# Kernel tuning notes

Measured on AMD Instinct MI355X. Metric: run time of the kernel, lower is better.

The kernel has to match this reference:

```python
import jax, jax.numpy as jnp
import numpy as np

EMBED_DIM = 1024
NUM_HEADS = 16
HEAD_DIM = EMBED_DIM // NUM_HEADS


def setup_inputs() -> dict:
    key = jax.random.key(0)
    ks = jax.random.split(key, 9)
    B, S, D = 4, 2048, EMBED_DIM
    s = 1.0 / np.sqrt(D)
    inp = {
        "x": jax.random.normal(ks[0], (B, S, D), dtype=jnp.float32),
        "Wq": jax.random.uniform(ks[1], (D, D), jnp.float32, -s, s),
        "bq": jax.random.uniform(ks[2], (D,), jnp.float32, -s, s),
        "Wk": jax.random.uniform(ks[3], (D, D), jnp.float32, -s, s),
        "bk": jax.random.uniform(ks[4], (D,), jnp.float32, -s, s),
        "Wv": jax.random.uniform(ks[5], (D, D), jnp.float32, -s, s),
        "bv": jax.random.uniform(ks[6], (D,), jnp.float32, -s, s),
        "Wo": jax.random.uniform(ks[7], (D, D), jnp.float32, -s, s),
        "bo": jax.random.uniform(ks[8], (D,), jnp.float32, -s, s),
    }
    return inp


def reference(x, Wq, bq, Wk, bk, Wv, bv, Wo, bo):
    B, S, D = x.shape
    H, Hd = NUM_HEADS, HEAD_DIM
    scale = 1.0 / jnp.sqrt(jnp.asarray(Hd, x.dtype))

    def split_heads(t):  # (B,S,D) -> (B,H,S,Hd)
        return t.reshape(B, S, H, Hd).transpose(0, 2, 1, 3)

    q = split_heads(x @ Wq + bq)
    k = split_heads(x @ Wk + bk)
    v = split_heads(x @ Wv + bv)

    scores = jnp.einsum("bhqd,bhkd->bhqk", q, k) * scale
    attn = jax.nn.softmax(scores, axis=-1)  # dropout is identity in eval mode
    out = jnp.einsum("bhqk,bhkd->bhqd", attn, v)
    out = out.transpose(0, 2, 1, 3).reshape(B, S, D)
    return out @ Wo + bo
```

## Files before the change

### kernel.cpp

```cpp
#include <hip/hip_runtime.h>
#include <cstdint>

typedef unsigned short u16;
typedef uint32_t u32;
typedef float f32x4 __attribute__((ext_vector_type(4)));
typedef short s16x8 __attribute__((ext_vector_type(8)));
typedef u16 u16x4 __attribute__((ext_vector_type(4)));
typedef u32 u32x2 __attribute__((ext_vector_type(2)));
typedef u32 u32x4 __attribute__((ext_vector_type(4)));

__device__ __forceinline__ u16 f2bf(float f) {
  u32 u = __builtin_bit_cast(u32, f);
  u += 0x7FFFu + ((u >> 16) & 1u);
  return (u16)(u >> 16);
}

__device__ __forceinline__ u32 pack2bf_trunc(float lo, float hi) {
  return __builtin_amdgcn_perm(__builtin_bit_cast(u32, hi),
                               __builtin_bit_cast(u32, lo), 0x07060302u);
}

template <typename T>
__device__ __forceinline__ T ldv(const void* p) {
  T v;
  __builtin_memcpy(&v, __builtin_assume_aligned(p, 16), sizeof(T));
  return v;
}

__device__ __forceinline__ void gload_lds16(const void* g, void* l) {
  __builtin_amdgcn_global_load_lds((const __attribute__((address_space(1))) void*)g,
                                   (__attribute__((address_space(3))) void*)l, 16, 0, 0);
}

__global__ __launch_bounds__(256) void cvt_x_k(const float* __restrict__ in,
                                               u16* __restrict__ out) {
  const int i = (blockIdx.x * 256 + threadIdx.x) * 4;
  float4 v = *(const float4*)(in + i);
  u16x4 o;
  o.x = f2bf(v.x); o.y = f2bf(v.y); o.z = f2bf(v.z); o.w = f2bf(v.w);
  *(u16x4*)(out + i) = o;
}

__global__ __launch_bounds__(256) void prep_w_k(const float* __restrict__ Wq,
                                                const float* __restrict__ Wk,
                                                const float* __restrict__ Wv,
                                                const float* __restrict__ Wo,
                                                u16* __restrict__ out) {
  __shared__ u16 t[64][72];
  const float* W = (blockIdx.z == 0) ? Wq : (blockIdx.z == 1) ? Wk
                  : (blockIdx.z == 2) ? Wv : Wo;
  u16* O = out + (size_t)blockIdx.z * 1024 * 1024;
  const int n0 = blockIdx.x * 64, k0 = blockIdx.y * 64;
  const int tid = threadIdx.x;
#pragma unroll
  for (int i = 0; i < 16; ++i) {
    int e = i * 256 + tid;
    int r = e >> 6, c = e & 63;
    t[r][c] = f2bf(W[(size_t)(k0 + r) * 1024 + n0 + c]);
  }
  __syncthreads();
#pragma unroll
  for (int i = 0; i < 16; ++i) {
    int e = i * 256 + tid;
    int rr = e >> 6, cc = e & 63;
    O[(size_t)(n0 + rr) * 1024 + k0 + cc] = t[cc][rr];
  }
}

__global__ __launch_bounds__(512, 2) void gemm_qkv_k(const u16* __restrict__ A,
                                                     const u16* __restrict__ Wt,
                                                     const float* __restrict__ bq,
                                                     const float* __restrict__ bk,
                                                     const float* __restrict__ bv,
                                                     u16* __restrict__ Qh,
                                                     u16* __restrict__ Kh,
                                                     u16* __restrict__ Vt,
                                                     float qscale) {
  constexpr int K = 1024;
  __shared__ __attribute__((aligned(16))) u16 As[2][256][64];
  __shared__ __attribute__((aligned(16))) u16 Bs[2][128][64];
  const int tid = threadIdx.x;
  const int l = tid & 63, w = tid >> 6;
  const int lr = l & 15, lg = l >> 4;
  const int m0 = blockIdx.x * 256;
  const int ng = blockIdx.y * 128;
  const int seg = ng >> 10;
  const int n0 = ng & 1023;
  const u16* Bt = Wt + ((size_t)seg << 20);
  const int wr = (w >> 1) * 64, wc = (w & 1) * 64;
  const int rT = tid >> 3;
  const int cSw = (((tid & 7) ^ ((tid >> 3) & 7)) << 3);

  f32x4 acc[4][4] = {};

#define GSTAGE(buf, kt)                                                         \
  do {                                                                          \
    _Pragma("unroll")                                                           \
    for (int i = 0; i < 4; ++i)                                                 \
      gload_lds16(A + (size_t)(m0 + i * 64 + rT) * K + (kt) + cSw,              \
                  &As[buf][i * 64][0] + (size_t)w * 512);                       \
    _Pragma("unroll")                                                           \
    for (int i = 0; i < 2; ++i)                                                 \
      gload_lds16(Bt + (size_t)(n0 + i * 64 + rT) * K + (kt) + cSw,             \
                  &Bs[buf][i * 64][0] + (size_t)w * 512);                       \
  } while (0)

  GSTAGE(0, 0);
  for (int ki = 0; ki < 16; ++ki) {
    const int cur = ki & 1;
    if (ki < 15) {
      GSTAGE(cur ^ 1, (ki + 1) * 64);
      asm volatile("s_waitcnt vmcnt(6)" ::: "memory");
    } else {
      asm volatile("s_waitcnt vmcnt(0)" ::: "memory");
    }
    __builtin_amdgcn_sched_barrier(0);
    __builtin_amdgcn_s_barrier();
    __builtin_amdgcn_sched_barrier(0);
#pragma unroll
    for (int kk = 0; kk < 2; ++kk) {
      s16x8 a[4], b[4];
#pragma unroll
      for (int mi = 0; mi < 4; ++mi)
        a[mi] = ldv<s16x8>(&As[cur][wr + mi * 16 + lr][((kk * 4 + lg) ^ (lr & 7)) << 3]);
#pragma unroll
      for (int ni = 0; ni < 4; ++ni)
        b[ni] = ldv<s16x8>(&Bs[cur][wc + ni * 16 + lr][((kk * 4 + lg) ^ (lr & 7)) << 3]);
#pragma unroll
      for (int mi = 0; mi < 4; ++mi)
#pragma unroll
        for (int ni = 0; ni < 4; ++ni)
          acc[mi][ni] = __builtin_amdgcn_mfma_f32_16x16x32_bf16(a[mi], b[ni], acc[mi][ni], 0, 0, 0);
    }
    __builtin_amdgcn_sched_barrier(0);
    __builtin_amdgcn_s_barrier();
  }
#undef GSTAGE

  const float* bias = (seg == 0) ? bq : (seg == 1) ? bk : bv;
  const float scale = (seg == 0) ? qscale : 1.0f;
  u16* outp = (seg == 0) ? Qh : (seg == 1) ? Kh : Vt;

  u16* Cb = &As[0][0][0];
  const int bb = m0 >> 11;
  const int sbase = m0 & 2047;

#pragma unroll
  for (int p = 0; p < 2; ++p) {
    __syncthreads();
    if ((wc >> 6) == p) {
#pragma unroll
      for (int ni = 0; ni < 4; ++ni) {
        const int c = ni * 16 + lr;
        const float bvv = bias[n0 + p * 64 + c];
#pragma unroll
        for (int mi = 0; mi < 4; ++mi) {
#pragma unroll
          for (int r = 0; r < 4; ++r) {
            const int row = wr + mi * 16 + lg * 4 + r;
            Cb[row * 64 + ((((c >> 3) ^ (row & 7)) << 3) | (c & 7))] =
                f2bf((acc[mi][ni][r] + bvv) * scale);
          }
        }
      }
    }
    __syncthreads();
    const int h = (n0 + p * 64) >> 6;
    if (seg <= 1) {
      const int row = tid >> 1;
      const int s = sbase + row;
#pragma unroll
      for (int j = 0; j < 4; ++j) {
        const int c = (tid & 1) * 32 + j * 8;
        s16x8 v = ldv<s16x8>(&Cb[row * 64 + (((c >> 3) ^ (row & 7)) << 3)]);
        const int chunk = (seg == 0) ? (c >> 3) : (((c >> 3) ^ (s & 7)) & 7);
        *(s16x8*)(outp + ((size_t)((bb << 4) + h) * 2048 + s) * 64 + (chunk << 3)) = v;
      }
    } else {
      const int hd = tid & 63;
#pragma unroll
      for (int j = 0; j < 4; ++j) {
        const int s0 = (tid >> 6) * 32 + j * 8;
        u16 vals[8];
#pragma unroll
        for (int i = 0; i < 8; ++i) {
          const int row = s0 + i;
          vals[i] = Cb[row * 64 + ((((hd >> 3) ^ (row & 7)) << 3) | (hd & 7))];
        }
        const int sl = sbase + s0;
        const int swz = (((sl >> 3) & 7) ^ (hd & 7)) & 7;
        *(s16x8*)(outp + ((size_t)((bb << 4) + h) * 64 + hd) * 2048 +
                  ((sl & ~63) | (swz << 3))) = *(s16x8*)vals;
      }
    }
  }
}

__global__ __launch_bounds__(512, 2) void gemm_o_k(const u16* __restrict__ A,
                                                   const u16* __restrict__ Bt,
                                                   const float* __restrict__ bias,
                                                   float* __restrict__ outp) {
  constexpr int K = 1024;
  __shared__ __attribute__((aligned(16))) u16 As[2][256][64];
  __shared__ __attribute__((aligned(16))) u16 Bs[2][128][64];
  const int tid = threadIdx.x;
  const int l = tid & 63, w = tid >> 6;
  const int lr = l & 15, lg = l >> 4;
  const int m0 = blockIdx.x * 256, n0 = blockIdx.y * 128;
  const int wr = (w >> 1) * 64, wc = (w & 1) * 64;
  const int rT = tid >> 3;
  const int cSw = (((tid & 7) ^ ((tid >> 3) & 7)) << 3);

  f32x4 acc[4][4] = {};

#define GSTAGE(buf, kt)                                                         \
  do {                                                                          \
    _Pragma("unroll")                                                           \
    for (int i = 0; i < 4; ++i)                                                 \
      gload_lds16(A + (size_t)(m0 + i * 64 + rT) * K + (kt) + cSw,              \
                  &As[buf][i * 64][0] + (size_t)w * 512);                       \
    _Pragma("unroll")                                                           \
    for (int i = 0; i < 2; ++i)                                                 \
      gload_lds16(Bt + (size_t)(n0 + i * 64 + rT) * K + (kt) + cSw,             \
                  &Bs[buf][i * 64][0] + (size_t)w * 512);                       \
  } while (0)

  GSTAGE(0, 0);
  for (int ki = 0; ki < 16; ++ki) {
    const int cur = ki & 1;
    if (ki < 15) {
      GSTAGE(cur ^ 1, (ki + 1) * 64);
      asm volatile("s_waitcnt vmcnt(6)" ::: "memory");
    } else {
      asm volatile("s_waitcnt vmcnt(0)" ::: "memory");
    }
    __builtin_amdgcn_sched_barrier(0);
    __builtin_amdgcn_s_barrier();
    __builtin_amdgcn_sched_barrier(0);
#pragma unroll
    for (int kk = 0; kk < 2; ++kk) {
      s16x8 a[4], b[4];
#pragma unroll
      for (int mi = 0; mi < 4; ++mi)
        a[mi] = ldv<s16x8>(&As[cur][wr + mi * 16 + lr][((kk * 4 + lg) ^ (lr & 7)) << 3]);
#pragma unroll
      for (int ni = 0; ni < 4; ++ni)
        b[ni] = ldv<s16x8>(&Bs[cur][wc + ni * 16 + lr][((kk * 4 + lg) ^ (lr & 7)) << 3]);
#pragma unroll
      for (int mi = 0; mi < 4; ++mi)
#pragma unroll
        for (int ni = 0; ni < 4; ++ni)
          acc[mi][ni] = __builtin_amdgcn_mfma_f32_16x16x32_bf16(a[mi], b[ni], acc[mi][ni], 0, 0, 0);
    }
    __builtin_amdgcn_sched_barrier(0);
    __builtin_amdgcn_s_barrier();
  }
#undef GSTAGE

#pragma unroll
  for (int ni = 0; ni < 4; ++ni) {
    const int col = n0 + wc + ni * 16 + lr;
    const float bv = bias[col];
#pragma unroll
    for (int mi = 0; mi < 4; ++mi)
#pragma unroll
      for (int r = 0; r < 4; ++r) {
        const int rowm = m0 + wr + mi * 16 + lg * 4 + r;
        outp[(size_t)rowm * 1024 + col] = acc[mi][ni][r] + bv;
      }
  }
}

__global__ __launch_bounds__(256, 4) void attn_k(const u16* __restrict__ Qh,
                                                 const u16* __restrict__ Kg,
                                                 const u16* __restrict__ Vg,
                                                 u16* __restrict__ Oattn) {
  __shared__ __attribute__((aligned(16))) u16 Kbuf[2][4096];
  __shared__ __attribute__((aligned(16))) u16 Vbuf[2][4096];
  __shared__ __attribute__((aligned(16))) u16 P_lds[4][16][64];
  const int tid = threadIdx.x, l = tid & 63, w = tid >> 6;
  const int lr = l & 15, lg = l >> 4;
  const int bh = blockIdx.y;
  const int q0 = blockIdx.x * 128 + w * 32;
  const u16* Q = Qh + (size_t)bh * (2048 * 64);
  const u16* K = Kg + (size_t)bh * (2048 * 64);
  const u16* V = Vg + (size_t)bh * (64 * 2048);

  s16x8 qf[2][2];
#pragma unroll
  for (int f = 0; f < 2; ++f)
#pragma unroll
    for (int kk = 0; kk < 2; ++kk)
      qf[f][kk] = ldv<s16x8>(Q + (size_t)(q0 + f * 16 + lr) * 64 + kk * 32 + lg * 8);

  const u32 one2 = 0x3F803F80u;
  const s16x8 onesv = __builtin_bit_cast(s16x8, (u32x4){one2, one2, one2, one2});

  f32x4 acc[2][4] = {};
  f32x4 lsum[2] = {};

#define STAGE(buf, kv0)                                                                 \
  do {                                                                                  \
    gload_lds16(K + (size_t)(kv0) * 64 + (size_t)tid * 8, &Kbuf[buf][w * 512]);         \
    gload_lds16(K + (size_t)(kv0) * 64 + 2048 + (size_t)tid * 8,                        \
                &Kbuf[buf][2048 + w * 512]);                                            \
    gload_lds16(V + (size_t)(tid >> 3) * 2048 + (kv0) + (tid & 7) * 8,                  \
                &Vbuf[buf][w * 512]);                                                   \
    gload_lds16(V + (size_t)((tid >> 3) + 32) * 2048 + (kv0) + (tid & 7) * 8,           \
                &Vbuf[buf][2048 + w * 512]);                                            \
  } while (0)

  STAGE(0, 0);

  for (int t = 0; t < 32; ++t) {
    const int cur = t & 1;
    if (t < 31) {
      STAGE(cur ^ 1, (t + 1) * 64);
      asm volatile("s_waitcnt vmcnt(4)" ::: "memory");
    } else {
      asm volatile("s_waitcnt vmcnt(0)" ::: "memory");
    }
    __builtin_amdgcn_sched_barrier(0);
    __builtin_amdgcn_s_barrier();
    __builtin_amdgcn_sched_barrier(0);

    f32x4 s[2][4] = {};
    __builtin_amdgcn_s_setprio(1);
#pragma unroll
    for (int tt = 0; tt < 4; ++tt) {
      s16x8 k0 = ldv<s16x8>(&Kbuf[cur][(tt * 16 + lr) * 64 + ((lg ^ (lr & 7)) << 3)]);
      s16x8 k1 = ldv<s16x8>(&Kbuf[cur][(tt * 16 + lr) * 64 + (((4 + lg) ^ (lr & 7)) << 3)]);
#pragma unroll
      for (int f = 0; f < 2; ++f) {
        s[f][tt] = __builtin_amdgcn_mfma_f32_16x16x32_bf16(k0, qf[f][0], s[f][tt], 0, 0, 0);
        s[f][tt] = __builtin_amdgcn_mfma_f32_16x16x32_bf16(k1, qf[f][1], s[f][tt], 0, 0, 0);
      }
    }
    __builtin_amdgcn_s_setprio(0);

    s16x8 pf[2][2];
#pragma unroll
    for (int f = 0; f < 2; ++f) {
#pragma unroll
      for (int tt = 0; tt < 4; ++tt)
#pragma unroll
        for (int r = 0; r < 4; ++r)
          s[f][tt][r] = __builtin_amdgcn_exp2f(s[f][tt][r]);
#pragma unroll
      for (int tt = 0; tt < 4; ++tt) {
        u32x2 pw;
        pw.x = pack2bf_trunc(s[f][tt][0], s[f][tt][1]);
        pw.y = pack2bf_trunc(s[f][tt][2], s[f][tt][3]);
        const int off = (((tt * 2 + (lg >> 1)) ^ (lr & 7)) << 3) + ((lg & 1) << 2);
        *(u32x2*)&P_lds[w][lr][off] = pw;
      }
#pragma unroll
      for (int kvc = 0; kvc < 2; ++kvc)
        pf[f][kvc] = ldv<s16x8>(&P_lds[w][lr][((kvc * 4 + lg) ^ (lr & 7)) << 3]);
      lsum[f] = __builtin_amdgcn_mfma_f32_16x16x32_bf16(pf[f][0], onesv, lsum[f], 0, 0, 0);
      lsum[f] = __builtin_amdgcn_mfma_f32_16x16x32_bf16(pf[f][1], onesv, lsum[f], 0, 0, 0);
    }

    __builtin_amdgcn_s_setprio(1);
#pragma unroll
    for (int dt = 0; dt < 4; ++dt) {
      s16x8 v0 = ldv<s16x8>(&Vbuf[cur][(dt * 16 + lr) * 64 + ((lg ^ (lr & 7)) << 3)]);
      s16x8 v1 = ldv<s16x8>(&Vbuf[cur][(dt * 16 + lr) * 64 + (((4 + lg) ^ (lr & 7)) << 3)]);
#pragma unroll
      for (int f = 0; f < 2; ++f) {
        acc[f][dt] = __builtin_amdgcn_mfma_f32_16x16x32_bf16(pf[f][0], v0, acc[f][dt], 0, 0, 0);
        acc[f][dt] = __builtin_amdgcn_mfma_f32_16x16x32_bf16(pf[f][1], v1, acc[f][dt], 0, 0, 0);
      }
    }
    __builtin_amdgcn_s_setprio(0);
    __builtin_amdgcn_sched_barrier(0);
    __builtin_amdgcn_s_barrier();
  }
#undef STAGE

  const int b = bh >> 4, h = bh & 15;
#pragma unroll
  for (int f = 0; f < 2; ++f) {
    float li[4];
#pragma unroll
    for (int r = 0; r < 4; ++r) li[r] = __builtin_amdgcn_rcpf(lsum[f][r]);
#pragma unroll
    for (int dt = 0; dt < 4; ++dt)
#pragma unroll
      for (int r = 0; r < 4; ++r) {
        const int q = q0 + f * 16 + lg * 4 + r;
        Oattn[(size_t)((b << 11) + q) * 1024 + (h << 6) + dt * 16 + lr] =
            f2bf(acc[f][dt][r] * li[r]);
      }
  }
}

extern "C" void kernel_launch(void* const* d_in, const int* in_sizes, int n_in,
                              void* d_out, int out_size, void* d_ws, size_t ws_size,
                              hipStream_t stream) {
  const float* x  = (const float*)d_in[0];
  const float* Wq = (const float*)d_in[1];
  const float* bq = (const float*)d_in[2];
  const float* Wk = (const float*)d_in[3];
  const float* bk = (const float*)d_in[4];
  const float* Wv = (const float*)d_in[5];
  const float* bv = (const float*)d_in[6];
  const float* Wo = (const float*)d_in[7];
  const float* bo = (const float*)d_in[8];

  char* ws = (char*)d_ws;
  const size_t MB = 1u << 20;
  u16* xb = (u16*)(ws);
  u16* wt = (u16*)(ws + 16 * MB);
  u16* Qh = (u16*)(ws + 24 * MB);
  u16* Kh = (u16*)(ws + 40 * MB);
  u16* Vt = (u16*)(ws + 56 * MB);
  u16* attn = xb;

  const float qscale = 0.125f * 1.44269504088896f;

  cvt_x_k<<<dim3(8192), dim3(256), 0, stream>>>(x, xb);
  prep_w_k<<<dim3(16, 16, 4), dim3(256), 0, stream>>>(Wq, Wk, Wv, Wo, wt);
  gemm_qkv_k<<<dim3(32, 24), dim3(512), 0, stream>>>(xb, wt, bq, bk, bv, Qh, Kh, Vt, qscale);
  attn_k<<<dim3(16, 64), dim3(256), 0, stream>>>(Qh, Kh, Vt, attn);
  gemm_o_k<<<dim3(32, 8), dim3(512), 0, stream>>>(attn, wt + 3 * 1048576, bo, (float*)d_out);
}
```

Before: 209.7 us.

## Unify QKV and output GEMMs into a 256x256-tile pipelined kernel

Replaces the separate QKV and output-projection GEMM kernels with one templated kernel using 256x256 output tiles per block. Global-to-LDS staging of A and B halves is interleaved with four quarter-steps of MFMA work, B is prefetched two stages ahead, and wave priority is raised around the MFMA groups. The goal is more operand reuse and better overlap of loads with compute. In exchange, LDS use doubles and accumulators grow, which can cut occupancy, and the output GEMM now launches only 128 blocks.

```diff
diff --git a/kernel.cpp b/kernel.cpp
--- a/kernel.cpp
+++ b/kernel.cpp
@@ -67,207 +67,177 @@
   }
 }
 
-__global__ __launch_bounds__(512, 2) void gemm_qkv_k(const u16* __restrict__ A,
-                                                     const u16* __restrict__ Wt,
-                                                     const float* __restrict__ bq,
-                                                     const float* __restrict__ bk,
-                                                     const float* __restrict__ bv,
-                                                     u16* __restrict__ Qh,
-                                                     u16* __restrict__ Kh,
-                                                     u16* __restrict__ Vt,
-                                                     float qscale) {
-  constexpr int K = 1024;
-  __shared__ __attribute__((aligned(16))) u16 As[2][256][64];
-  __shared__ __attribute__((aligned(16))) u16 Bs[2][128][64];
+template <int OMODE>
+__global__ __launch_bounds__(512, 2) void gemm8p_k(const u16* __restrict__ A,
+                                                   const u16* __restrict__ Wt,
+                                                   const float* __restrict__ bq,
+                                                   const float* __restrict__ bk,
+                                                   const float* __restrict__ bv,
+                                                   u16* __restrict__ Qh,
+                                                   u16* __restrict__ Kh,
+                                                   u16* __restrict__ Vt,
+                                                   float* __restrict__ Oo,
+                                                   float qscale) {
+  __shared__ __attribute__((aligned(16))) u16 As[2][2][128][64];
+  __shared__ __attribute__((aligned(16))) u16 Bs[2][2][128][64];
   const int tid = threadIdx.x;
   const int l = tid & 63, w = tid >> 6;
   const int lr = l & 15, lg = l >> 4;
+  const int wm = w >> 2, wn = w & 3;
   const int m0 = blockIdx.x * 256;
-  const int ng = blockIdx.y * 128;
-  const int seg = ng >> 10;
-  const int n0 = ng & 1023;
+  int seg, n0;
+  if constexpr (OMODE == 0) { seg = blockIdx.y >> 2; n0 = (blockIdx.y & 3) * 256; }
+  else { seg = 3; n0 = blockIdx.y * 256; }
   const u16* Bt = Wt + ((size_t)seg << 20);
-  const int wr = (w >> 1) * 64, wc = (w & 1) * 64;
   const int rT = tid >> 3;
-  const int cSw = (((tid & 7) ^ ((tid >> 3) & 7)) << 3);
-
-  f32x4 acc[4][4] = {};
-
-#define GSTAGE(buf, kt)                                                         \
+  const int cSw = (((tid & 7) ^ (rT & 7)) << 3);
+  const int xk = lr & 7;
+
+  f32x4 acc[8][4] = {};
+  s16x8 bfr[4][2];
+
+#define STG_A(buf, h, kt)                                                       \
   do {                                                                          \
-    _Pragma("unroll")                                                           \
-    for (int i = 0; i < 4; ++i)                                                 \
-      gload_lds16(A + (size_t)(m0 + i * 64 + rT) * K + (kt) + cSw,              \
-                  &As[buf][i * 64][0] + (size_t)w * 512);                       \
-    _Pragma("unroll")                                                           \
-    for (int i = 0; i < 2; ++i)                                                 \
-      gload_lds16(Bt + (size_t)(n0 + i * 64 + rT) * K + (kt) + cSw,             \
-                  &Bs[buf][i * 64][0] + (size_t)w * 512);                       \
+    gload_lds16(A + (size_t)(m0 + (h) * 128 + rT) * 1024 + (kt) + cSw,          \
+                &As[buf][h][0][0] + w * 512);                                   \
+    gload_lds16(A + (size_t)(m0 + (h) * 128 + 64 + rT) * 1024 + (kt) + cSw,     \
+                &As[buf][h][64][0] + w * 512);                                  \
   } while (0)
-
-  GSTAGE(0, 0);
-  for (int ki = 0; ki < 16; ++ki) {
-    const int cur = ki & 1;
-    if (ki < 15) {
-      GSTAGE(cur ^ 1, (ki + 1) * 64);
-      asm volatile("s_waitcnt vmcnt(6)" ::: "memory");
-    } else {
-      asm volatile("s_waitcnt vmcnt(0)" ::: "memory");
-    }
-    __builtin_amdgcn_sched_barrier(0);
-    __builtin_amdgcn_s_barrier();
-    __builtin_amdgcn_sched_barrier(0);
-#pragma unroll
-    for (int kk = 0; kk < 2; ++kk) {
-      s16x8 a[4], b[4];
-#pragma unroll
-      for (int mi = 0; mi < 4; ++mi)
-        a[mi] = ldv<s16x8>(&As[cur][wr + mi * 16 + lr][((kk * 4 + lg) ^ (lr & 7)) << 3]);
-#pragma unroll
-      for (int ni = 0; ni < 4; ++ni)
-        b[ni] = ldv<s16x8>(&Bs[cur][wc + ni * 16 + lr][((kk * 4 + lg) ^ (lr & 7)) << 3]);
-#pragma unroll
-      for (int mi = 0; mi < 4; ++mi)
+#define STG_B(buf, h, kt)                                                       \
+  do {                                                                          \
+    gload_lds16(Bt + (size_t)(n0 + (h) * 128 + rT) * 1024 + (kt) + cSw,         \
+                &Bs[buf][h][0][0] + w * 512);                                   \
+    gload_lds16(Bt + (size_t)(n0 + (h) * 128 + 64 + rT) * 1024 + (kt) + cSw,    \
+                &Bs[buf][h][64][0] + w * 512);                                  \
+  } while (0)
+
+  STG_B(0, 0, 0); STG_B(0, 1, 0);
+  STG_A(0, 0, 0); STG_A(0, 1, 0);
+  STG_B(1, 0, 64); STG_B(1, 1, 64);
+  asm volatile("s_waitcnt vmcnt(4)" ::: "memory");
+  __builtin_amdgcn_sched_barrier(0);
+  __builtin_amdgcn_s_barrier();
+  __builtin_amdgcn_sched_barrier(0);
+
+#pragma unroll 2
+  for (int t = 0; t < 16; ++t) {
+    const int cur = t & 1;
+    const int kt1 = (t + 1) * 64, kt2 = (t + 2) * 64;
+#pragma unroll
+    for (int q = 0; q < 4; ++q) {
+      s16x8 aq[2][2];
+#pragma unroll
+      for (int sub = 0; sub < 2; ++sub)
+#pragma unroll
+        for (int kk = 0; kk < 2; ++kk)
+          aq[sub][kk] = ldv<s16x8>(
+              &As[cur][wm][q * 32 + sub * 16 + lr][((kk * 4 + lg) ^ xk) << 3]);
+      if (q == 0) {
 #pragma unroll
         for (int ni = 0; ni < 4; ++ni)
-          acc[mi][ni] = __builtin_amdgcn_mfma_f32_16x16x32_bf16(a[mi], b[ni], acc[mi][ni], 0, 0, 0);
-    }
-    __builtin_amdgcn_sched_barrier(0);
-    __builtin_amdgcn_s_barrier();
-  }
-#undef GSTAGE
-
-  const float* bias = (seg == 0) ? bq : (seg == 1) ? bk : bv;
-  const float scale = (seg == 0) ? qscale : 1.0f;
-  u16* outp = (seg == 0) ? Qh : (seg == 1) ? Kh : Vt;
-
-  u16* Cb = &As[0][0][0];
-  const int bb = m0 >> 11;
-  const int sbase = m0 & 2047;
-
-#pragma unroll
-  for (int p = 0; p < 2; ++p) {
-    __syncthreads();
-    if ((wc >> 6) == p) {
-#pragma unroll
-      for (int ni = 0; ni < 4; ++ni) {
-        const int c = ni * 16 + lr;
-        const float bvv = bias[n0 + p * 64 + c];
-#pragma unroll
-        for (int mi = 0; mi < 4; ++mi) {
-#pragma unroll
-          for (int r = 0; r < 4; ++r) {
-            const int row = wr + mi * 16 + lg * 4 + r;
-            Cb[row * 64 + ((((c >> 3) ^ (row & 7)) << 3) | (c & 7))] =
-                f2bf((acc[mi][ni][r] + bvv) * scale);
+#pragma unroll
+          for (int kk = 0; kk < 2; ++kk)
+            bfr[ni][kk] = ldv<s16x8>(
+                &Bs[cur][wn >> 1][(wn & 1) * 64 + ni * 16 + lr][((kk * 4 + lg) ^ xk) << 3]);
+      }
+      if (q == 0)      { if (t < 15) STG_A(cur ^ 1, 0, kt1); }
+      else if (q == 1) { if (t < 15) STG_A(cur ^ 1, 1, kt1); }
+      else if (q == 2) { if (t < 14) STG_B(cur, 0, kt2); }
+      else             { if (t < 14) STG_B(cur, 1, kt2); }
+      __builtin_amdgcn_sched_barrier(0);
+      __builtin_amdgcn_s_barrier();
+      __builtin_amdgcn_sched_barrier(0);
+      __builtin_amdgcn_s_setprio(1);
+#pragma unroll
+      for (int kk = 0; kk < 2; ++kk)
+#pragma unroll
+        for (int sub = 0; sub < 2; ++sub)
+#pragma unroll
+          for (int ni = 0; ni < 4; ++ni)
+            acc[q * 2 + sub][ni] = __builtin_amdgcn_mfma_f32_16x16x32_bf16(
+                aq[sub][kk], bfr[ni][kk], acc[q * 2 + sub][ni], 0, 0, 0);
+      __builtin_amdgcn_s_setprio(0);
+      if (q == 3) {
+        if (t < 14) asm volatile("s_waitcnt vmcnt(4)" ::: "memory");
+        else        asm volatile("s_waitcnt vmcnt(0)" ::: "memory");
+      }
+      __builtin_amdgcn_sched_barrier(0);
+      __builtin_amdgcn_s_barrier();
+      __builtin_amdgcn_sched_barrier(0);
+    }
+  }
+#undef STG_A
+#undef STG_B
+
+  if constexpr (OMODE == 1) {
+#pragma unroll
+    for (int ni = 0; ni < 4; ++ni) {
+      const int col = n0 + wn * 64 + ni * 16 + lr;
+      const float bvv = bq[col];
+#pragma unroll
+      for (int mi = 0; mi < 8; ++mi)
+#pragma unroll
+        for (int r = 0; r < 4; ++r) {
+          const int row = m0 + wm * 128 + mi * 16 + lg * 4 + r;
+          Oo[(size_t)row * 1024 + col] = acc[mi][ni][r] + bvv;
+        }
+    }
+    return;
+  } else {
+    const float* bias = (seg == 0) ? bq : (seg == 1) ? bk : bv;
+    const float scale = (seg == 0) ? qscale : 1.0f;
+    u16* outp = (seg == 0) ? Qh : (seg == 1) ? Kh : Vt;
+    u16* Cb = &As[0][0][0][0];
+    const int bb = m0 >> 11;
+    const int sbase = m0 & 2047;
+#pragma unroll
+    for (int p = 0; p < 4; ++p) {
+      __syncthreads();
+      if (wn == p) {
+#pragma unroll
+        for (int ni = 0; ni < 4; ++ni) {
+          const int c = ni * 16 + lr;
+          const float bvv = bias[n0 + p * 64 + c];
+#pragma unroll
+          for (int mi = 0; mi < 8; ++mi)
+#pragma unroll
+            for (int r = 0; r < 4; ++r) {
+              const int row = wm * 128 + mi * 16 + lg * 4 + r;
+              Cb[row * 64 + ((((c >> 3) ^ (row & 7)) << 3) | (c & 7))] =
+                  f2bf((acc[mi][ni][r] + bvv) * scale);
+            }
+        }
+      }
+      __syncthreads();
+      const int h = (n0 + p * 64) >> 6;
+      if (seg <= 1) {
+        const int row = tid >> 1;
+        const int s = sbase + row;
+#pragma unroll
+        for (int j = 0; j < 4; ++j) {
+          const int c = (tid & 1) * 32 + j * 8;
+          s16x8 v = ldv<s16x8>(&Cb[row * 64 + (((c >> 3) ^ (row & 7)) << 3)]);
+          const int chunk = (seg == 0) ? (c >> 3) : (((c >> 3) ^ (s & 7)) & 7);
+          *(s16x8*)(outp + ((size_t)((bb << 4) + h) * 2048 + s) * 64 + (chunk << 3)) = v;
+        }
+      } else {
+        const int hd = tid & 63;
+#pragma unroll
+        for (int j = 0; j < 4; ++j) {
+          const int s0 = (tid >> 6) * 32 + j * 8;
+          u16 vals[8];
+#pragma unroll
+          for (int i = 0; i < 8; ++i) {
+            const int row = s0 + i;
+            vals[i] = Cb[row * 64 + ((((hd >> 3) ^ (row & 7)) << 3) | (hd & 7))];
           }
+          const int sl = sbase + s0;
+          const int swz = (((sl >> 3) & 7) ^ (hd & 7)) & 7;
+          *(s16x8*)(outp + ((size_t)((bb << 4) + h) * 64 + hd) * 2048 +
+                    ((sl & ~63) | (swz << 3))) = *(s16x8*)vals;
         }
       }
     }
-    __syncthreads();
-    const int h = (n0 + p * 64) >> 6;
-    if (seg <= 1) {
-      const int row = tid >> 1;
-      const int s = sbase + row;
-#pragma unroll
-      for (int j = 0; j < 4; ++j) {
-        const int c = (tid & 1) * 32 + j * 8;
-        s16x8 v = ldv<s16x8>(&Cb[row * 64 + (((c >> 3) ^ (row & 7)) << 3)]);
-        const int chunk = (seg == 0) ? (c >> 3) : (((c >> 3) ^ (s & 7)) & 7);
-        *(s16x8*)(outp + ((size_t)((bb << 4) + h) * 2048 + s) * 64 + (chunk << 3)) = v;
-      }
-    } else {
-      const int hd = tid & 63;
-#pragma unroll
-      for (int j = 0; j < 4; ++j) {
-        const int s0 = (tid >> 6) * 32 + j * 8;
-        u16 vals[8];
-#pragma unroll
-        for (int i = 0; i < 8; ++i) {
-          const int row = s0 + i;
-          vals[i] = Cb[row * 64 + ((((hd >> 3) ^ (row & 7)) << 3) | (hd & 7))];
-        }
-        const int sl = sbase + s0;
-        const int swz = (((sl >> 3) & 7) ^ (hd & 7)) & 7;
-        *(s16x8*)(outp + ((size_t)((bb << 4) + h) * 64 + hd) * 2048 +
-                  ((sl & ~63) | (swz << 3))) = *(s16x8*)vals;
-      }
-    }
-  }
-}
-
-__global__ __launch_bounds__(512, 2) void gemm_o_k(const u16* __restrict__ A,
-                                                   const u16* __restrict__ Bt,
-                                                   const float* __restrict__ bias,
-                                                   float* __restrict__ outp) {
-  constexpr int K = 1024;
-  __shared__ __attribute__((aligned(16))) u16 As[2][256][64];
-  __shared__ __attribute__((aligned(16))) u16 Bs[2][128][64];
-  const int tid = threadIdx.x;
-  const int l = tid & 63, w = tid >> 6;
-  const int lr = l & 15, lg = l >> 4;
-  const int m0 = blockIdx.x * 256, n0 = blockIdx.y * 128;
-  const int wr = (w >> 1) * 64, wc = (w & 1) * 64;
-  const int rT = tid >> 3;
-  const int cSw = (((tid & 7) ^ ((tid >> 3) & 7)) << 3);
-
-  f32x4 acc[4][4] = {};
-
-#define GSTAGE(buf, kt)                                                         \
-  do {                                                                          \
-    _Pragma("unroll")                                                           \
-    for (int i = 0; i < 4; ++i)                                                 \
-      gload_lds16(A + (size_t)(m0 + i * 64 + rT) * K + (kt) + cSw,              \
-                  &As[buf][i * 64][0] + (size_t)w * 512);                       \
-    _Pragma("unroll")                                                           \
-    for (int i = 0; i < 2; ++i)                                                 \
-      gload_lds16(Bt + (size_t)(n0 + i * 64 + rT) * K + (kt) + cSw,             \
-                  &Bs[buf][i * 64][0] + (size_t)w * 512);                       \
-  } while (0)
-
-  GSTAGE(0, 0);
-  for (int ki = 0; ki < 16; ++ki) {
-    const int cur = ki & 1;
-    if (ki < 15) {
-      GSTAGE(cur ^ 1, (ki + 1) * 64);
-      asm volatile("s_waitcnt vmcnt(6)" ::: "memory");
-    } else {
-      asm volatile("s_waitcnt vmcnt(0)" ::: "memory");
-    }
-    __builtin_amdgcn_sched_barrier(0);
-    __builtin_amdgcn_s_barrier();
-    __builtin_amdgcn_sched_barrier(0);
-#pragma unroll
-    for (int kk = 0; kk < 2; ++kk) {
-      s16x8 a[4], b[4];
-#pragma unroll
-      for (int mi = 0; mi < 4; ++mi)
-        a[mi] = ldv<s16x8>(&As[cur][wr + mi * 16 + lr][((kk * 4 + lg) ^ (lr & 7)) << 3]);
-#pragma unroll
-      for (int ni = 0; ni < 4; ++ni)
-        b[ni] = ldv<s16x8>(&Bs[cur][wc + ni * 16 + lr][((kk * 4 + lg) ^ (lr & 7)) << 3]);
-#pragma unroll
-      for (int mi = 0; mi < 4; ++mi)
-#pragma unroll
-        for (int ni = 0; ni < 4; ++ni)
-          acc[mi][ni] = __builtin_amdgcn_mfma_f32_16x16x32_bf16(a[mi], b[ni], acc[mi][ni], 0, 0, 0);
-    }
-    __builtin_amdgcn_sched_barrier(0);
-    __builtin_amdgcn_s_barrier();
-  }
-#undef GSTAGE
-
-#pragma unroll
-  for (int ni = 0; ni < 4; ++ni) {
-    const int col = n0 + wc + ni * 16 + lr;
-    const float bv = bias[col];
-#pragma unroll
-    for (int mi = 0; mi < 4; ++mi)
-#pragma unroll
-      for (int r = 0; r < 4; ++r) {
-        const int rowm = m0 + wr + mi * 16 + lg * 4 + r;
-        outp[(size_t)rowm * 1024 + col] = acc[mi][ni][r] + bv;
-      }
   }
 }
 
@@ -421,7 +391,10 @@
 
   cvt_x_k<<<dim3(8192), dim3(256), 0, stream>>>(x, xb);
   prep_w_k<<<dim3(16, 16, 4), dim3(256), 0, stream>>>(Wq, Wk, Wv, Wo, wt);
-  gemm_qkv_k<<<dim3(32, 24), dim3(512), 0, stream>>>(xb, wt, bq, bk, bv, Qh, Kh, Vt, qscale);
+  gemm8p_k<0><<<dim3(32, 12), dim3(512), 0, stream>>>(xb, wt, bq, bk, bv, Qh, Kh, Vt,
+                                                      nullptr, qscale);
   attn_k<<<dim3(16, 64), dim3(256), 0, stream>>>(Qh, Kh, Vt, attn);
-  gemm_o_k<<<dim3(32, 8), dim3(512), 0, stream>>>(attn, wt + 3 * 1048576, bo, (float*)d_out);
-}
+  gemm8p_k<1><<<dim3(32, 4), dim3(512), 0, stream>>>(attn, wt, bo, nullptr, nullptr,
+                                                     nullptr, nullptr, nullptr,
+                                                     (float*)d_out, 1.0f);
+}
```

New measurement: 229.2 us. +9.3%, slower.
